# Optimization experiments

Hardware: AMD Instinct MI355X
Metric: run time of the kernel (lower is better)

## Reference

```python
import jax, jax.numpy as jnp
import numpy as np

B_ = 2; L_ = 4096; D_MODEL = 1024; D_INNER = 2048; D_STATE = 128
N_HEADS = 32; HEADDIM = 64; D_CONV = 4; CHUNK = 64
CONV_DIM = D_INNER + 2 * D_STATE
EPS = 1e-5


def silu(x):
    return x * jax.nn.sigmoid(x)


def segsum(x):
    # x: (..., T) -> (..., T, T) stable segment sums; exp() gives 1-semiseparable matrix
    T = x.shape[-1]
    xe = jnp.broadcast_to(x[..., None], x.shape + (T,))  # (..., T, T)
    lower = jnp.tril(jnp.ones((T, T), bool), -1)
    xs = jnp.cumsum(jnp.where(lower, xe, 0.0), axis=-2)
    incl = jnp.tril(jnp.ones((T, T), bool), 0)
    return jnp.where(incl, xs, -jnp.inf)


def ssd(x, A, Bm, Cm):
    # x: (b, l, h, p); A: (b, l, h); Bm/Cm: (b, l, n) (single shared head, as in module)
    b, l, h, p = x.shape
    c = l // CHUNK
    x = x.reshape(b, c, CHUNK, h, p)
    A = A.reshape(b, c, CHUNK, h).transpose(0, 3, 1, 2)  # (b, h, c, l)
    Bm = Bm.reshape(b, c, CHUNK, D_STATE)
    Cm = Cm.reshape(b, c, CHUNK, D_STATE)
    A_cumsum = jnp.cumsum(A, axis=-1)                    # (b, h, c, l)
    Lmat = jnp.exp(segsum(A))                            # (b, h, c, l, l)
    # intra-chunk (diagonal blocks)
    Y_diag = jnp.einsum('bcln,bcsn,bhcls,bcshp->bclhp', Cm, Bm, Lmat, x)
    # per-chunk states
    decay_states = jnp.exp(A_cumsum[:, :, :, -1:] - A_cumsum)  # (b, h, c, l)
    states = jnp.einsum('bcln,bhcl,bclhp->bchpn', Bm, decay_states, x)
    init = jnp.zeros_like(states[:, :1])
    states = jnp.concatenate([init, states], axis=1)     # (b, c+1, h, p, n)
    A_last = jnp.pad(A_cumsum[:, :, :, -1], ((0, 0), (0, 0), (1, 0)))  # (b, h, c+1)
    decay_chunk = jnp.exp(segsum(A_last))                # (b, h, c+1, c+1)
    new_states = jnp.einsum('bhzc,bchpn->bzhpn', decay_chunk, states)
    states_prev = new_states[:, :-1]                     # (b, c, h, p, n)
    state_decay_out = jnp.exp(A_cumsum)
    Y_off = jnp.einsum('bcln,bchpn,bhcl->bclhp', Cm, states_prev, state_decay_out)
    return (Y_diag + Y_off).reshape(b, l, h, p)


def setup_inputs() -> dict:
    key = jax.random.key(0)
    ks = jax.random.split(key, 9)
    u = jax.random.normal(ks[0], (B_, L_, D_MODEL), jnp.float32)
    W_in = jax.random.normal(ks[1], (2 * D_INNER + 2 * D_STATE + N_HEADS, D_MODEL), jnp.float32) * (D_MODEL ** -0.5)
    conv_w = jax.random.normal(ks[2], (CONV_DIM, 1, D_CONV), jnp.float32) * 0.2
    conv_b = jax.random.normal(ks[3], (CONV_DIM,), jnp.float32) * 0.02
    dt_bias = jax.random.normal(ks[4], (N_HEADS,), jnp.float32) * 0.1
    A_log = jnp.log(jax.random.uniform(ks[5], (N_HEADS,), jnp.float32, 1.0, 16.0))
    D_param = jax.random.normal(ks[6], (N_HEADS,), jnp.float32) * 0.5
    norm_w = jnp.ones((D_INNER,), jnp.float32)
    W_out = jax.random.normal(ks[7], (D_MODEL, D_INNER), jnp.float32) * (D_INNER ** -0.5)
    return dict(u=u, W_in=W_in, conv_w=conv_w, conv_b=conv_b, dt_bias=dt_bias,
                A_log=A_log, D_param=D_param, norm_w=norm_w, W_out=W_out)


def mamba_forward(u, W_in, conv_w, conv_b, dt_bias, A_log, D_param, norm_w, W_out):
    b, l, _ = u.shape
    zxbcdt = u @ W_in.T                                  # (b, l, 2*di+2*ds+h)
    z = zxbcdt[..., :D_INNER]
    xBC = zxbcdt[..., D_INNER:D_INNER + CONV_DIM]
    dt = zxbcdt[..., D_INNER + CONV_DIM:]
    dt = jax.nn.softplus(dt + dt_bias)                   # (b, l, h)
    # causal depthwise conv1d
    xc = jnp.transpose(xBC, (0, 2, 1))                   # (b, conv_dim, l)
    xc = jax.lax.conv_general_dilated(xc, conv_w, (1,), [(D_CONV - 1, 0)],
                                      feature_group_count=CONV_DIM,
                                      dimension_numbers=('NCH', 'OIH', 'NCH'))
    xc = xc + conv_b[None, :, None]
    xBC = silu(jnp.transpose(xc, (0, 2, 1)))             # (b, l, conv_dim)
    x = xBC[..., :D_INNER]
    Bc = xBC[..., D_INNER:D_INNER + D_STATE]
    Cc = xBC[..., D_INNER + D_STATE:]
    x = x.reshape(b, l, N_HEADS, HEADDIM)
    A = -jnp.exp(A_log)                                  # (h,)
    Y = ssd(x * dt[..., None], A * dt, Bc, Cc)           # (b, l, h, p)
    y = Y + x * D_param[:, None]
    y = y.reshape(b, l, D_INNER)
    # gated RMSNorm
    y = y * silu(z)
    y = y * jax.lax.rsqrt(jnp.mean(y * y, axis=-1, keepdims=True) + EPS) * norm_w
    return y @ W_out.T


def reference(u, W_in, conv_w, conv_b, dt_bias, A_log, D_param, norm_w, W_out):
    return mamba_forward(u, W_in, conv_w, conv_b, dt_bias, A_log, D_param, norm_w, W_out)
```

## Files before the change

### kernel.cpp

```cpp
#include <hip/hip_runtime.h>
#include <hip/hip_bf16.h>
#include <math.h>

#define B_    2
#define L_    4096
#define DM    1024
#define DI    2048
#define DS    128
#define NH    32
#define HD    64
#define CHUNK 64
#define NC    (L_/CHUNK)
#define CD    (DI + 2*DS)
#define ROWS  (B_*L_)
#define NOUT  (2*DI + 2*DS + NH)
#define NPAD2 4608

typedef __attribute__((ext_vector_type(4))) float f32x4;
typedef __attribute__((ext_vector_type(8))) __bf16 bf16x8;
typedef __attribute__((ext_vector_type(4))) short s16x4;
typedef __attribute__((ext_vector_type(8))) short s16x8;

__global__ __launch_bounds__(256) void k_convert_all(const float* __restrict__ u, const float* __restrict__ W_in,
                                                     const float* __restrict__ W_out, __bf16* __restrict__ ubf,
                                                     __bf16* __restrict__ wibf, __bf16* __restrict__ wobf) {
    int i = blockIdx.x * 256 + threadIdx.x;
    const int QU  = ROWS * DM / 4;
    const int QWI = NPAD2 * DM / 4;
    const int QWO = DM * DI / 4;
    const float* s = nullptr;
    __bf16* d;
    bool zero = false;
    if (i < QU) {
        s = u + (size_t)i * 4; d = ubf + (size_t)i * 4;
    } else if (i < QU + QWI) {
        int j = i - QU;
        d = wibf + (size_t)j * 4;
        if (j < NOUT * DM / 4) s = W_in + (size_t)j * 4; else zero = true;
    } else if (i < QU + QWI + QWO) {
        int j = i - QU - QWI;
        s = W_out + (size_t)j * 4; d = wobf + (size_t)j * 4;
    } else return;
    s16x4 o = {0, 0, 0, 0};
    if (!zero) {
        f32x4 v = *(const f32x4*)s;
#pragma unroll
        for (int q = 0; q < 4; q++) o[q] = __builtin_bit_cast(short, (__bf16)v[q]);
    }
    *(s16x4*)d = o;
}

__device__ __forceinline__ void stage_half(const __bf16* __restrict__ G, int ldg, int grow0, int kt,
                                           char* lds, int ldsoff, int tid, int wave) {
#pragma unroll
    for (int issue = 0; issue < 2; issue++) {
        int o   = issue * 8192 + tid * 16;
        int row = o >> 7;
        int cb  = (o & 127) ^ ((row & 7) << 4);
        const __bf16* src = G + (size_t)(grow0 + row) * ldg + kt + (cb >> 1);
        char* ldsbase = lds + ldsoff + issue * 8192 + wave * 1024;
        __builtin_amdgcn_global_load_lds((const __attribute__((address_space(1))) void*)src,
                                         (__attribute__((address_space(3))) void*)ldsbase,
                                         16, 0, 0);
    }
}

__device__ __forceinline__ bf16x8 rdfrag(const char* lds, int ldsoff, int r, int ks, int lane) {
    int logical = r * 128 + ks * 64 + ((lane >> 4) << 4);
    int phys    = logical ^ ((r & 7) << 4);
    return *(const bf16x8*)(lds + ldsoff + phys);
}

__device__ __forceinline__ void gemm128x128_core(const __bf16* __restrict__ Ag, const __bf16* __restrict__ Bg,
                                                 int K, int m0, int n0, char* lds, f32x4 acc[4][2]) {
    const int tid = threadIdx.x, wave = tid >> 6, lane = tid & 63;
    const int wm = wave >> 2, wn = wave & 3, lrow = lane & 15;
    const int KT = K >> 6;

    for (int t = 0; t < KT; t++) {
        const int kt = t << 6;
        stage_half(Ag, K, m0, kt, lds, 0,     tid, wave);
        stage_half(Bg, K, n0, kt, lds, 16384, tid, wave);
        asm volatile("s_waitcnt vmcnt(0)" ::: "memory");
        __builtin_amdgcn_s_barrier();
        bf16x8 a[4][2];
#pragma unroll
        for (int fm = 0; fm < 4; fm++)
#pragma unroll
            for (int ks = 0; ks < 2; ks++)
                a[fm][ks] = rdfrag(lds, 0, wm * 64 + fm * 16 + lrow, ks, lane);
        __builtin_amdgcn_s_setprio(1);
#pragma unroll
        for (int fn = 0; fn < 2; fn++) {
            bf16x8 b0 = rdfrag(lds, 16384, wn * 32 + fn * 16 + lrow, 0, lane);
            bf16x8 b1 = rdfrag(lds, 16384, wn * 32 + fn * 16 + lrow, 1, lane);
#pragma unroll
            for (int fm = 0; fm < 4; fm++) {
                acc[fm][fn] = __builtin_amdgcn_mfma_f32_16x16x32_bf16(a[fm][0], b0, acc[fm][fn], 0, 0, 0);
                acc[fm][fn] = __builtin_amdgcn_mfma_f32_16x16x32_bf16(a[fm][1], b1, acc[fm][fn], 0, 0, 0);
            }
        }
        __builtin_amdgcn_s_setprio(0);
        __builtin_amdgcn_s_barrier();
    }
}

__global__ __launch_bounds__(512, 4) void k_gemm1(const __bf16* __restrict__ ubf, const __bf16* __restrict__ wibf,
                                                  __bf16* __restrict__ zbuf, __bf16* __restrict__ xbcraw,
                                                  float* __restrict__ dtbuf, const float* __restrict__ dt_bias) {
    extern __shared__ char lds[];
    f32x4 acc[4][2];
    f32x4 z4 = {0.f, 0.f, 0.f, 0.f};
#pragma unroll
    for (int i = 0; i < 4; i++)
#pragma unroll
        for (int j = 0; j < 2; j++) acc[i][j] = z4;

    int bid = blockIdx.x;
    int wg  = (bid & 7) * 280 + (bid >> 3);
    int m0  = (wg / 35) * 128;
    int n0  = (wg % 35) * 128;
    gemm128x128_core(ubf, wibf, DM, m0, n0, lds, acc);

    const int lane = threadIdx.x & 63, wave = threadIdx.x >> 6;
    const int wm = wave >> 2, wn = wave & 3;
    const int gm_base = m0 + wm * 64 + ((lane >> 4) << 2);
    const int gn_base = n0 + wn * 32 + (lane & 15);
#pragma unroll
    for (int fm = 0; fm < 4; fm++) {
        const int gmb = gm_base + fm * 16;
#pragma unroll
        for (int fn = 0; fn < 2; fn++) {
            const int gn = gn_base + fn * 16;
            if (gn < DI) {
#pragma unroll
                for (int r = 0; r < 4; r++)
                    zbuf[(size_t)(gmb + r) * DI + gn] = (__bf16)acc[fm][fn][r];
            } else if (gn < DI + CD) {
#pragma unroll
                for (int r = 0; r < 4; r++)
                    xbcraw[(size_t)(gmb + r) * CD + (gn - DI)] = (__bf16)acc[fm][fn][r];
            } else if (gn < NOUT) {
                const int hh = gn - (DI + CD);
                const float bb = dt_bias[hh];
#pragma unroll
                for (int r = 0; r < 4; r++) {
                    float x = acc[fm][fn][r] + bb;
                    float sp = (x > 20.f) ? x : log1pf(__expf(x));
                    dtbuf[(size_t)(gmb + r) * NH + hh] = sp;
                }
            }
        }
    }
}

__global__ __launch_bounds__(512, 4) void k_gemm2(const __bf16* __restrict__ ybf, const __bf16* __restrict__ wobf,
                                                  float* __restrict__ out) {
    extern __shared__ char lds[];
    f32x4 acc[4][2];
    f32x4 z4 = {0.f, 0.f, 0.f, 0.f};
#pragma unroll
    for (int i = 0; i < 4; i++)
#pragma unroll
        for (int j = 0; j < 2; j++) acc[i][j] = z4;

    int bid = blockIdx.x;
    int wg  = (bid & 7) * 64 + (bid >> 3);
    int m0  = (wg / 8) * 128;
    int n0  = (wg % 8) * 128;
    gemm128x128_core(ybf, wobf, DI, m0, n0, lds, acc);

    const int lane = threadIdx.x & 63, wave = threadIdx.x >> 6;
    const int wm = wave >> 2, wn = wave & 3;
    const int gm_base = m0 + wm * 64 + ((lane >> 4) << 2);
    const int gn_base = n0 + wn * 32 + (lane & 15);
#pragma unroll
    for (int fm = 0; fm < 4; fm++) {
        const int gmb = gm_base + fm * 16;
#pragma unroll
        for (int fn = 0; fn < 2; fn++) {
            const int gn = gn_base + fn * 16;
#pragma unroll
            for (int r = 0; r < 4; r++)
                out[(size_t)(gmb + r) * DM + gn] = acc[fm][fn][r];
        }
    }
}

__global__ __launch_bounds__(256) void k_conv(const __bf16* __restrict__ xbcraw, const float* __restrict__ conv_w,
                                              const float* __restrict__ conv_b, __bf16* __restrict__ xconv) {
    __shared__ float wsh[256 * 4];
    __shared__ float bsh[256];
    const int tid  = threadIdx.x;
    const int gsub = tid & 31;
    const int roct = tid >> 5;
    const int ch_base_blk = blockIdx.x * 256;
    *(f32x4*)&wsh[tid * 4] = *(const f32x4*)&conv_w[ch_base_blk * 4 + tid * 4];
    bsh[tid] = conv_b[ch_base_blk + tid];
    __syncthreads();

    const int ch0  = ch_base_blk + gsub * 8;
    const int row0 = (blockIdx.y * 8 + roct) * 8;
    const int l0   = row0 & (L_ - 1);
    const __bf16* src = xbcraw + (size_t)row0 * CD + ch0;

    s16x8 rr[11];
#pragma unroll
    for (int j = 0; j < 11; j++) {
        int ll = l0 - 3 + j;
        if (ll >= 0) rr[j] = *(const s16x8*)(src + (size_t)(j - 3) * CD);
        else         rr[j] = (s16x8){0, 0, 0, 0, 0, 0, 0, 0};
    }

    const int chl = gsub * 8;
    float w[8][4], bias[8];
#pragma unroll
    for (int j = 0; j < 8; j++) {
        bias[j] = bsh[chl + j];
#pragma unroll
        for (int k = 0; k < 4; k++) w[j][k] = wsh[(chl + j) * 4 + k];
    }

    __bf16* dst = xconv + (size_t)row0 * CD + ch0;
#pragma unroll
    for (int orow = 0; orow < 8; orow++) {
        float a[8];
#pragma unroll
        for (int j = 0; j < 8; j++) a[j] = bias[j];
#pragma unroll
        for (int k = 0; k < 4; k++) {
            s16x8 v = rr[orow + k];
#pragma unroll
            for (int j = 0; j < 8; j++)
                a[j] += w[j][k] * (float)__builtin_bit_cast(__bf16, (short)v[j]);
        }
        s16x8 o;
#pragma unroll
        for (int j = 0; j < 8; j++)
            o[j] = __builtin_bit_cast(short, (__bf16)(a[j] * __builtin_amdgcn_rcpf(1.f + __expf(-a[j]))));
        *(s16x8*)(dst + (size_t)orow * CD) = o;
    }
}

__global__ __launch_bounds__(256) void k_cbt(const __bf16* __restrict__ xconv, float* __restrict__ cbt) {
    const int c = blockIdx.x, b = blockIdx.y;
    const int tid = threadIdx.x, wv = tid >> 6, lane = tid & 63;
    const int lrow = lane & 15, lko = (lane >> 4) * 8;
    __shared__ __align__(16) __bf16 Csh[64 * 136];
    __shared__ __align__(16) __bf16 Bsh[64 * 136];
    const size_t rowbase = (size_t)b * L_ + c * CHUNK;
#pragma unroll
    for (int q = 0; q < 32; q++) {
        int i = q * 2 + (wv >> 1);
        int n = (wv & 1) * 64 + lane;
        const __bf16* base = xconv + (rowbase + i) * CD + DI;
        Bsh[i * 136 + n] = base[n];
        Csh[i * 136 + n] = base[DS + n];
    }
    __syncthreads();
    f32x4 acc[4];
    f32x4 z4 = {0.f, 0.f, 0.f, 0.f};
#pragma unroll
    for (int jt = 0; jt < 4; jt++) acc[jt] = z4;
#pragma unroll
    for (int ks = 0; ks < 4; ks++) {
        bf16x8 a = *(const bf16x8*)&Csh[(wv * 16 + lrow) * 136 + ks * 32 + lko];
#pragma unroll
        for (int jt = 0; jt < 4; jt++) {
            bf16x8 bb = *(const bf16x8*)&Bsh[(jt * 16 + lrow) * 136 + ks * 32 + lko];
            acc[jt] = __builtin_amdgcn_mfma_f32_16x16x32_bf16(a, bb, acc[jt], 0, 0, 0);
        }
    }
    float* o = cbt + (size_t)(b * NC + c) * 4096;
#pragma unroll
    for (int jt = 0; jt < 4; jt++)
#pragma unroll
        for (int r = 0; r < 4; r++) {
            int i = wv * 16 + (lane >> 4) * 4 + r;
            int j = jt * 16 + lrow;
            o[i * 64 + j] = acc[jt][r];
        }
}

__global__ __launch_bounds__(256) void k_ssd_a(const __bf16* __restrict__ xconv, const float* __restrict__ dtbuf,
                                               const float* __restrict__ A_log,
                                               __bf16* __restrict__ states, float* __restrict__ asum) {
    const int h = blockIdx.x, c = blockIdx.y, b = blockIdx.z;
    const int tid = threadIdx.x, wv = tid >> 6, lane = tid & 63;
    const int lrow = lane & 15, lko = (lane >> 4) * 8;
    __shared__ __align__(16) __bf16 xT[64 * 72];
    __shared__ __align__(16) __bf16 xsc[64 * 72];
    __shared__ __align__(16) __bf16 BT[128 * 72];
    __shared__ float dts[64], cum[64];

    const float Ah = -__expf(A_log[h]);
    const size_t rowbase = (size_t)b * L_ + c * CHUNK;

    float dtv = 0.f;
    if (wv == 0) { dtv = dtbuf[(rowbase + lane) * NH + h]; dts[lane] = dtv; }
#pragma unroll
    for (int q = 0; q < 16; q++) {
        int i = q * 4 + wv;
        xT[lane * 72 + i] = xconv[(rowbase + i) * CD + h * HD + lane];
    }
#pragma unroll
    for (int q = 0; q < 32; q++) {
        int i = q * 2 + (wv >> 1);
        int n = (wv & 1) * 64 + lane;
        BT[n * 72 + i] = xconv[(rowbase + i) * CD + DI + n];
    }
    if (wv == 0) {
        float v = Ah * dtv;
#pragma unroll
        for (int o = 1; o < 64; o <<= 1) { float t = __shfl_up(v, o); if (lane >= o) v += t; }
        cum[lane] = v;
        if (lane == 63) asum[(b * NC + c) * NH + h] = v;
    }
    __syncthreads();

    const float cum63 = cum[63];
#pragma unroll
    for (int q = 0; q < 16; q++) {
        int i = q * 4 + wv;
        float dcfi = __expf(cum63 - cum[i]) * dts[i];
        xsc[lane * 72 + i] = (__bf16)((float)xT[lane * 72 + i] * dcfi);
    }
    __syncthreads();

    f32x4 z4 = {0.f, 0.f, 0.f, 0.f};
    f32x4 accS[8];
#pragma unroll
    for (int nt = 0; nt < 8; nt++) accS[nt] = z4;
#pragma unroll
    for (int ks = 0; ks < 2; ks++) {
        bf16x8 a = *(const bf16x8*)&xsc[(wv * 16 + lrow) * 72 + ks * 32 + lko];
#pragma unroll
        for (int nt = 0; nt < 8; nt++) {
            bf16x8 bb = *(const bf16x8*)&BT[(nt * 16 + lrow) * 72 + ks * 32 + lko];
            accS[nt] = __builtin_amdgcn_mfma_f32_16x16x32_bf16(a, bb, accS[nt], 0, 0, 0);
        }
    }
    __bf16* sp = states + ((size_t)(b * NC + c) * NH + h) * 8192;
#pragma unroll
    for (int nt = 0; nt < 8; nt++)
#pragma unroll
        for (int r = 0; r < 4; r++) {
            int p = wv * 16 + (lane >> 4) * 4 + r;
            int n = nt * 16 + lrow;
            sp[p * 128 + n] = (__bf16)accS[nt][r];
        }
}

__global__ __launch_bounds__(256) void k_scan(__bf16* __restrict__ states, const float* __restrict__ asum) {
    const int seg = blockIdx.x, h = blockIdx.y, b = blockIdx.z;
    __shared__ float efs[NC];
    if (threadIdx.x < NC) efs[threadIdx.x] = __expf(asum[(b * NC + threadIdx.x) * NH + h]);
    __syncthreads();
    const int e0 = seg * 1024 + threadIdx.x * 4;
    __bf16* base = states + ((size_t)(b * NC) * NH + h) * 8192 + e0;
    const size_t cs = (size_t)NH * 8192;
    float S[4] = {0.f, 0.f, 0.f, 0.f};
    s16x4 r0 = *(const s16x4*)(base);
    s16x4 r1 = *(const s16x4*)(base + cs);
    s16x4 r2 = *(const s16x4*)(base + 2 * cs);
    s16x4 r3;
#define SCAN_STEP(RV, CC)                                                                  \
    {                                                                                      \
        s16x4 o; float e = efs[CC];                                                        \
        _Pragma("unroll")                                                                  \
        for (int q = 0; q < 4; q++) {                                                      \
            float t = (float)__builtin_bit_cast(__bf16, (short)RV[q]);                     \
            o[q] = __builtin_bit_cast(short, (__bf16)S[q]);                                \
            S[q] = e * S[q] + t;                                                           \
        }                                                                                  \
        *(s16x4*)(base + (size_t)(CC) * cs) = o;                                           \
    }
    for (int c = 0; c < NC; c += 4) {
        r3 = *(const s16x4*)(base + (size_t)(c + 3) * cs);
        SCAN_STEP(r0, c);
        if (c + 4 < NC) r0 = *(const s16x4*)(base + (size_t)(c + 4) * cs);
        SCAN_STEP(r1, c + 1);
        if (c + 5 < NC) r1 = *(const s16x4*)(base + (size_t)(c + 5) * cs);
        SCAN_STEP(r2, c + 2);
        if (c + 6 < NC) r2 = *(const s16x4*)(base + (size_t)(c + 6) * cs);
        SCAN_STEP(r3, c + 3);
    }
#undef SCAN_STEP
}

__global__ __launch_bounds__(256) void k_ssd_b(const __bf16* __restrict__ xconv, const float* __restrict__ dtbuf,
                                               const __bf16* __restrict__ states, const float* __restrict__ A_log,
                                               const float* __restrict__ cbt, const float* __restrict__ D_param,
                                               __bf16* __restrict__ ybuf) {
    const int h = blockIdx.x, c = blockIdx.y, b = blockIdx.z;
    const int tid = threadIdx.x, wv = tid >> 6, lane = tid & 63;
    const int lrow = lane & 15, lko = (lane >> 4) * 8;
    __shared__ __align__(16) __bf16 xT[64 * 72];
    __shared__ __align__(16) __bf16 Ms[64 * 72];
    __shared__ __align__(16) __bf16 Csh[64 * 136];
    __shared__ __align__(16) __bf16 Sps[64 * 136];
    __shared__ float dts[64], cum[64];

    const float Ah = -__expf(A_log[h]);
    const size_t rowbase = (size_t)b * L_ + c * CHUNK;
    const __bf16* sp = states + ((size_t)(b * NC + c) * NH + h) * 8192;
#pragma unroll
    for (int q = 0; q < 32; q++) {
        int i = q * 2 + (wv >> 1);
        int n = (wv & 1) * 64 + lane;
        Csh[i * 136 + n] = xconv[(rowbase + i) * CD + DI + DS + n];
        Sps[i * 136 + n] = sp[i * 128 + n];
    }
#pragma unroll
    for (int q = 0; q < 16; q++) {
        int i = q * 4 + wv;
        xT[lane * 72 + i] = xconv[(rowbase + i) * CD + h * HD + lane];
    }
    if (wv == 0) {
        float dtv = dtbuf[(rowbase + lane) * NH + h];
        dts[lane] = dtv;
        float v = Ah * dtv;
#pragma unroll
        for (int o = 1; o < 64; o <<= 1) { float t = __shfl_up(v, o); if (lane >= o) v += t; }
        cum[lane] = v;
    }
    __syncthreads();

    const float Dh = D_param[h];
    const float* cbt_bc = cbt + (size_t)(b * NC + c) * 4096;
#pragma unroll
    for (int q = 0; q < 16; q++) {
        int i = q * 4 + wv, j = lane;
        float m = 0.f;
        if (j <= i) m = cbt_bc[i * 64 + j] * __expf(cum[i] - cum[j]) * dts[j];
        if (j == i) m += Dh;
        Ms[i * 72 + j] = (__bf16)m;
    }
    __syncthreads();

    f32x4 z4 = {0.f, 0.f, 0.f, 0.f};
    f32x4 accY[4], accO[4];
#pragma unroll
    for (int pt = 0; pt < 4; pt++) { accY[pt] = z4; accO[pt] = z4; }
#pragma unroll
    for (int ks = 0; ks < 2; ks++) {
        bf16x8 a = *(const bf16x8*)&Ms[(wv * 16 + lrow) * 72 + ks * 32 + lko];
#pragma unroll
        for (int pt = 0; pt < 4; pt++) {
            bf16x8 bb = *(const bf16x8*)&xT[(pt * 16 + lrow) * 72 + ks * 32 + lko];
            accY[pt] = __builtin_amdgcn_mfma_f32_16x16x32_bf16(a, bb, accY[pt], 0, 0, 0);
        }
    }
#pragma unroll
    for (int ks = 0; ks < 4; ks++) {
        bf16x8 a = *(const bf16x8*)&Csh[(wv * 16 + lrow) * 136 + ks * 32 + lko];
#pragma unroll
        for (int pt = 0; pt < 4; pt++) {
            bf16x8 bb = *(const bf16x8*)&Sps[(pt * 16 + lrow) * 136 + ks * 32 + lko];
            accO[pt] = __builtin_amdgcn_mfma_f32_16x16x32_bf16(a, bb, accO[pt], 0, 0, 0);
        }
    }
#pragma unroll
    for (int r = 0; r < 4; r++) {
        int i = wv * 16 + (lane >> 4) * 4 + r;
        float ef = __expf(cum[i]);
#pragma unroll
        for (int pt = 0; pt < 4; pt++) {
            size_t idx = (rowbase + i) * DI + h * HD + pt * 16 + lrow;
            ybuf[idx] = (__bf16)(accY[pt][r] + ef * accO[pt][r]);
        }
    }
}

__global__ __launch_bounds__(256) void k_gate_norm(const __bf16* __restrict__ ybuf, const __bf16* __restrict__ zbuf,
                                                   const float* __restrict__ norm_w, __bf16* __restrict__ ybf) {
    const int r = blockIdx.x;
    const int tid = threadIdx.x;
    const int col0 = tid * 8;
    s16x8 y8 = *(const s16x8*)(ybuf + (size_t)r * DI + col0);
    s16x8 z8 = *(const s16x8*)(zbuf + (size_t)r * DI + col0);
    float v[8];
    float ss = 0.f;
#pragma unroll
    for (int q = 0; q < 8; q++) {
        float y = (float)__builtin_bit_cast(__bf16, (short)y8[q]);
        float z = (float)__builtin_bit_cast(__bf16, (short)z8[q]);
        float g = z * __builtin_amdgcn_rcpf(1.f + __expf(-z));
        v[q] = y * g;
        ss += v[q] * v[q];
    }
#pragma unroll
    for (int o = 32; o > 0; o >>= 1) ss += __shfl_down(ss, o);
    __shared__ float wsum[4];
    __shared__ float rmss;
    if ((tid & 63) == 0) wsum[tid >> 6] = ss;
    __syncthreads();
    if (tid == 0) {
        float t = wsum[0] + wsum[1] + wsum[2] + wsum[3];
        rmss = rsqrtf(t / (float)DI + 1e-5f);
    }
    __syncthreads();
    float rm = rmss;
    s16x8 o8;
#pragma unroll
    for (int q = 0; q < 8; q++)
        o8[q] = __builtin_bit_cast(short, (__bf16)(v[q] * rm * norm_w[col0 + q]));
    *(s16x8*)(ybf + (size_t)r * DI + col0) = o8;
}

extern "C" void kernel_launch(void* const* d_in, const int* in_sizes, int n_in,
                              void* d_out, int out_size, void* d_ws, size_t ws_size,
                              hipStream_t stream) {
    const float* u       = (const float*)d_in[0];
    const float* W_in    = (const float*)d_in[1];
    const float* conv_w  = (const float*)d_in[2];
    const float* conv_b  = (const float*)d_in[3];
    const float* dt_bias = (const float*)d_in[4];
    const float* A_log   = (const float*)d_in[5];
    const float* D_param = (const float*)d_in[6];
    const float* norm_w  = (const float*)d_in[7];
    const float* W_out   = (const float*)d_in[8];
    float* out = (float*)d_out;

    constexpr size_t OFF_WOBF  = 0;
    constexpr size_t OFF_ZBUF  = 4194304;
    constexpr size_t OFF_DT    = 37748736;
    constexpr size_t OFF_ASUM  = 38797312;
    constexpr size_t OFF_XCONV = 38813696;
    constexpr size_t OFF_CBT   = 76562432;
    constexpr size_t OFF_BIG   = 78659584;
    constexpr size_t NEED      = 145768448;
    if (ws_size < NEED) return;

    char* ws = (char*)d_ws;
    __bf16* wobf   = (__bf16*)(ws + OFF_WOBF);
    __bf16* zbuf   = (__bf16*)(ws + OFF_ZBUF);
    float*  dtbuf  = (float*) (ws + OFF_DT);
    float*  asum   = (float*) (ws + OFF_ASUM);
    __bf16* xconv  = (__bf16*)(ws + OFF_XCONV);
    float*  cbt    = (float*) (ws + OFF_CBT);
    __bf16* ubf    = (__bf16*)(ws + OFF_BIG);
    __bf16* wibf   = (__bf16*)(ws + OFF_BIG + 16777216);
    __bf16* xbcraw = (__bf16*)(ws + OFF_BIG + 16777216 + 9437184);
    __bf16* states = (__bf16*)(ws + OFF_BIG);
    __bf16* ybf    = (__bf16*)(ws + OFF_XCONV);
    __bf16* ybuf   = (__bf16*)d_out;

    (void)hipFuncSetAttribute((const void*)k_gemm1, hipFuncAttributeMaxDynamicSharedMemorySize, 32768);
    (void)hipFuncSetAttribute((const void*)k_gemm2, hipFuncAttributeMaxDynamicSharedMemorySize, 32768);

    constexpr int QTOT = ROWS * DM / 4 + NPAD2 * DM / 4 + DM * DI / 4;
    k_convert_all<<<(QTOT + 255) / 256, 256, 0, stream>>>(u, W_in, W_out, ubf, wibf, wobf);

    k_gemm1<<<2240, 512, 32768, stream>>>(ubf, wibf, zbuf, xbcraw, dtbuf, dt_bias);
    k_conv<<<dim3(9, 128), 256, 0, stream>>>(xbcraw, conv_w, conv_b, xconv);
    k_cbt<<<dim3(NC, B_), 256, 0, stream>>>(xconv, cbt);
    k_ssd_a<<<dim3(NH, NC, B_), 256, 0, stream>>>(xconv, dtbuf, A_log, states, asum);
    k_scan<<<dim3(8, NH, B_), 256, 0, stream>>>(states, asum);
    k_ssd_b<<<dim3(NH, NC, B_), 256, 0, stream>>>(xconv, dtbuf, states, A_log, cbt, D_param, ybuf);
    k_gate_norm<<<ROWS, 256, 0, stream>>>(ybuf, zbuf, norm_w, ybf);
    k_gemm2<<<512, 512, 32768, stream>>>(ybf, wobf, out);
}
```

Before: 299.6 us.

## Fuse gated RMSNorm into output GEMM A-tile staging

Adds a GEMM kernel that reads y and z directly, applies the SiLU gate and norm weight while staging the A tile into LDS, accumulates per-row sums of squares, and scales the output by the per-row rsqrt after the K loop. This removes the separate gate-norm kernel launch and the bf16 round trip of the normalized activations. It adds recomputation of the gate in each of the 8 column tiles per row block and pulls the global loads into the synchronous staging path. It needs a larger workspace and falls back to the old path otherwise.

New measurement: 330.4 us. 10.3% more time.

```diff
diff --git a/kernel.cpp b/kernel.cpp
--- a/kernel.cpp
+++ b/kernel.cpp
@@ -187,6 +187,110 @@
     }
 }
 
+__global__ __launch_bounds__(512, 4) void k_gemm2f(const __bf16* __restrict__ ybuf, const __bf16* __restrict__ zbuf,
+                                                   const float* __restrict__ norm_w, const __bf16* __restrict__ wobf,
+                                                   float* __restrict__ out) {
+    extern __shared__ char lds[];
+    const int tid = threadIdx.x, wave = tid >> 6, lane = tid & 63;
+    const int wm = wave >> 2, wn = wave & 3, lrow = lane & 15;
+
+    f32x4 acc[4][2];
+    f32x4 z4 = {0.f, 0.f, 0.f, 0.f};
+#pragma unroll
+    for (int i = 0; i < 4; i++)
+#pragma unroll
+        for (int j = 0; j < 2; j++) acc[i][j] = z4;
+
+    int bid = blockIdx.x;
+    int wg  = (bid & 7) * 64 + (bid >> 3);
+    int m0  = (wg / 8) * 128;
+    int n0  = (wg % 8) * 128;
+
+    const int rA = tid >> 3;
+    float ssA = 0.f, ssB = 0.f;
+
+    for (int t = 0; t < 32; t++) {
+        const int kt = t << 6;
+        stage_half(wobf, DI, n0, kt, lds, 16384, tid, wave);
+#pragma unroll
+        for (int issue = 0; issue < 2; issue++) {
+            const int o    = issue * 8192 + tid * 16;
+            const int row  = o >> 7;
+            const int colb = o & 127;
+            const int col  = kt + (colb >> 1);
+            const __bf16* yp = ybuf + (size_t)(m0 + row) * DI + col;
+            const __bf16* zp = zbuf + (size_t)(m0 + row) * DI + col;
+            s16x8 y8 = *(const s16x8*)yp;
+            s16x8 z8 = *(const s16x8*)zp;
+            f32x4 nw0 = *(const f32x4*)(norm_w + col);
+            f32x4 nw1 = *(const f32x4*)(norm_w + col + 4);
+            float ssl = 0.f;
+            s16x8 a8;
+#pragma unroll
+            for (int j = 0; j < 8; j++) {
+                float y = (float)__builtin_bit_cast(__bf16, (short)y8[j]);
+                float z = (float)__builtin_bit_cast(__bf16, (short)z8[j]);
+                float g = y * z * __builtin_amdgcn_rcpf(1.f + __expf(-z));
+                ssl += g * g;
+                float nw = (j < 4) ? nw0[j] : nw1[j - 4];
+                a8[j] = __builtin_bit_cast(short, (__bf16)(g * nw));
+            }
+            if (issue == 0) ssA += ssl; else ssB += ssl;
+            const int phys = (row << 7) | (colb ^ ((row & 7) << 4));
+            *(s16x8*)(lds + phys) = a8;
+        }
+        asm volatile("s_waitcnt vmcnt(0) lgkmcnt(0)" ::: "memory");
+        __builtin_amdgcn_s_barrier();
+        bf16x8 a[4][2];
+#pragma unroll
+        for (int fm = 0; fm < 4; fm++)
+#pragma unroll
+            for (int ks = 0; ks < 2; ks++)
+                a[fm][ks] = rdfrag(lds, 0, wm * 64 + fm * 16 + lrow, ks, lane);
+        __builtin_amdgcn_s_setprio(1);
+#pragma unroll
+        for (int fn = 0; fn < 2; fn++) {
+            bf16x8 b0 = rdfrag(lds, 16384, wn * 32 + fn * 16 + lrow, 0, lane);
+            bf16x8 b1 = rdfrag(lds, 16384, wn * 32 + fn * 16 + lrow, 1, lane);
+#pragma unroll
+            for (int fm = 0; fm < 4; fm++) {
+                acc[fm][fn] = __builtin_amdgcn_mfma_f32_16x16x32_bf16(a[fm][0], b0, acc[fm][fn], 0, 0, 0);
+                acc[fm][fn] = __builtin_amdgcn_mfma_f32_16x16x32_bf16(a[fm][1], b1, acc[fm][fn], 0, 0, 0);
+            }
+        }
+        __builtin_amdgcn_s_setprio(0);
+        __builtin_amdgcn_s_barrier();
+    }
+
+#pragma unroll
+    for (int off = 1; off < 8; off <<= 1) {
+        ssA += __shfl_xor(ssA, off);
+        ssB += __shfl_xor(ssB, off);
+    }
+    float* rmsh = (float*)(lds + 32768);
+    if ((tid & 7) == 0) {
+        rmsh[rA]      = rsqrtf(ssA * (1.f / (float)DI) + 1e-5f);
+        rmsh[64 + rA] = rsqrtf(ssB * (1.f / (float)DI) + 1e-5f);
+    }
+    __syncthreads();
+
+    const int gm_base = m0 + wm * 64 + ((lane >> 4) << 2);
+    const int gn_base = n0 + wn * 32 + (lane & 15);
+#pragma unroll
+    for (int fm = 0; fm < 4; fm++) {
+        const int gmb = gm_base + fm * 16;
+#pragma unroll
+        for (int fn = 0; fn < 2; fn++) {
+            const int gn = gn_base + fn * 16;
+#pragma unroll
+            for (int r = 0; r < 4; r++) {
+                float rms = rmsh[gmb + r - m0];
+                out[(size_t)(gmb + r) * DM + gn] = acc[fm][fn][r] * rms;
+            }
+        }
+    }
+}
+
 __global__ __launch_bounds__(256) void k_conv(const __bf16* __restrict__ xbcraw, const float* __restrict__ conv_w,
                                               const float* __restrict__ conv_b, __bf16* __restrict__ xconv) {
     __shared__ float wsh[256 * 4];
@@ -530,7 +634,10 @@
     constexpr size_t OFF_CBT   = 76562432;
     constexpr size_t OFF_BIG   = 78659584;
     constexpr size_t NEED      = 145768448;
+    constexpr size_t OFF_YB2   = 145768448;
+    constexpr size_t NEED2     = 179322880;
     if (ws_size < NEED) return;
+    const bool fused = (ws_size >= NEED2);
 
     char* ws = (char*)d_ws;
     __bf16* wobf   = (__bf16*)(ws + OFF_WOBF);
@@ -544,10 +651,12 @@
     __bf16* xbcraw = (__bf16*)(ws + OFF_BIG + 16777216 + 9437184);
     __bf16* states = (__bf16*)(ws + OFF_BIG);
     __bf16* ybf    = (__bf16*)(ws + OFF_XCONV);
-    __bf16* ybuf   = (__bf16*)d_out;
-
-    (void)hipFuncSetAttribute((const void*)k_gemm1, hipFuncAttributeMaxDynamicSharedMemorySize, 32768);
-    (void)hipFuncSetAttribute((const void*)k_gemm2, hipFuncAttributeMaxDynamicSharedMemorySize, 32768);
+    __bf16* ybuf   = fused ? (__bf16*)(ws + OFF_YB2)
+                           : (__bf16*)d_out;
+
+    (void)hipFuncSetAttribute((const void*)k_gemm1,  hipFuncAttributeMaxDynamicSharedMemorySize, 32768);
+    (void)hipFuncSetAttribute((const void*)k_gemm2,  hipFuncAttributeMaxDynamicSharedMemorySize, 32768);
+    (void)hipFuncSetAttribute((const void*)k_gemm2f, hipFuncAttributeMaxDynamicSharedMemorySize, 33280);
 
     constexpr int QTOT = ROWS * DM / 4 + NPAD2 * DM / 4 + DM * DI / 4;
     k_convert_all<<<(QTOT + 255) / 256, 256, 0, stream>>>(u, W_in, W_out, ubf, wibf, wobf);
@@ -558,6 +667,10 @@
     k_ssd_a<<<dim3(NH, NC, B_), 256, 0, stream>>>(xconv, dtbuf, A_log, states, asum);
     k_scan<<<dim3(8, NH, B_), 256, 0, stream>>>(states, asum);
     k_ssd_b<<<dim3(NH, NC, B_), 256, 0, stream>>>(xconv, dtbuf, states, A_log, cbt, D_param, ybuf);
-    k_gate_norm<<<ROWS, 256, 0, stream>>>(ybuf, zbuf, norm_w, ybf);
-    k_gemm2<<<512, 512, 32768, stream>>>(ybf, wobf, out);
-}
+    if (fused) {
+        k_gemm2f<<<512, 512, 33280, stream>>>(ybuf, zbuf, norm_w, wobf, out);
+    } else {
+        k_gate_norm<<<ROWS, 256, 0, stream>>>(ybuf, zbuf, norm_w, ybf);
+        k_gemm2<<<512, 512, 32768, stream>>>(ybf, wobf, out);
+    }
+}
```
